# Optimization experiments

Measured on AMD Instinct MI355X. Metric: run time of the kernel, lower is better.

## Reference

```python
import jax, jax.numpy as jnp
import numpy as np

N_NODES = 100000
N_EDGES = 1600000
IN_FEATS, N_HIDDEN, N_CLASSES = 128, 128, 40


def _sage_layer(h, src, dst, W_self, W_neigh, b):
    # DGL SAGEConv (mean): fc_self(h) + fc_neigh(mean_{u in N_in(v)} h_u)
    msg = h[src]  # [E, F] gather of source-node features
    summed = jax.ops.segment_sum(msg, dst, num_segments=N_NODES)  # [N, F]
    deg = jax.ops.segment_sum(jnp.ones((src.shape[0], 1), h.dtype), dst,
                              num_segments=N_NODES)  # [N, 1] in-degree
    h_neigh = summed / jnp.maximum(deg, 1.0)
    return h @ W_self + b + h_neigh @ W_neigh


def setup_inputs() -> dict:
    key = jax.random.key(0)
    ks = jax.random.split(key, 12)
    inputs = jax.random.normal(ks[0], (N_NODES, IN_FEATS), dtype=jnp.float32)
    src = jax.random.randint(ks[1], (N_EDGES,), 0, N_NODES, dtype=jnp.int64)
    dst = jax.random.randint(ks[2], (N_EDGES,), 0, N_NODES, dtype=jnp.int64)

    def lin(k, fi, fo):
        return jax.random.normal(k, (fi, fo), dtype=jnp.float32) / np.sqrt(fi)

    return {
        "inputs": inputs, "src": src, "dst": dst,
        "W_self0": lin(ks[3], IN_FEATS, N_HIDDEN),
        "W_neigh0": lin(ks[4], IN_FEATS, N_HIDDEN),
        "b0": jnp.zeros((N_HIDDEN,), jnp.float32),
        "W_self1": lin(ks[5], N_HIDDEN, N_HIDDEN),
        "W_neigh1": lin(ks[6], N_HIDDEN, N_HIDDEN),
        "b1": jnp.zeros((N_HIDDEN,), jnp.float32),
        "W_self2": lin(ks[7], N_HIDDEN, N_CLASSES),
        "W_neigh2": lin(ks[8], N_HIDDEN, N_CLASSES),
        "b2": jnp.zeros((N_CLASSES,), jnp.float32),
    }


def reference(inputs, src, dst, W_self0, W_neigh0, b0, W_self1, W_neigh1, b1,
              W_self2, W_neigh2, b2):
    # dropout p=0.0 -> identity
    h = _sage_layer(inputs, src, dst, W_self0, W_neigh0, b0)
    h = jax.nn.relu(h)
    h = _sage_layer(h, src, dst, W_self1, W_neigh1, b1)
    h = jax.nn.relu(h)
    h = _sage_layer(h, src, dst, W_self2, W_neigh2, b2)
    return h
```

## Files before the change

### kernel.cpp

```cpp
#include <hip/hip_runtime.h>


#define F_IN 128
#define SCAN_CHUNK 1024

typedef __attribute__((ext_vector_type(8))) short bf16x8;
typedef __attribute__((ext_vector_type(4))) float f32x4;

__device__ __forceinline__ unsigned short f32_to_bf16_rne(float x) {
    unsigned int u = __float_as_uint(x);
    unsigned int r = u + 0x7FFFu + ((u >> 16) & 1u);
    return (unsigned short)(r >> 16);
}
__device__ __forceinline__ float bf16_bits_to_f32(unsigned short h) {
    return __uint_as_float(((unsigned int)h) << 16);
}


__global__ __launch_bounds__(256) void count_deg_kernel(
    const int* __restrict__ dst, int* __restrict__ cnt, int E) {
    int i = blockIdx.x * 256 + threadIdx.x;
    if (i < E) atomicAdd(&cnt[dst[i]], 1);
}

__global__ __launch_bounds__(256) void scan_part1(
    const int* __restrict__ cnt, int* __restrict__ bsum, int n) {
    __shared__ int red[4];
    int base = blockIdx.x * SCAN_CHUNK + threadIdx.x * 4;
    int s = 0;
    if (base + 4 <= n) {
        int4 v = *(const int4*)&cnt[base];
        s = v.x + v.y + v.z + v.w;
    } else {
        for (int j = 0; j < 4; ++j) if (base + j < n) s += cnt[base + j];
    }
    for (int off = 32; off > 0; off >>= 1) s += __shfl_down(s, off, 64);
    if ((threadIdx.x & 63) == 0) red[threadIdx.x >> 6] = s;
    __syncthreads();
    if (threadIdx.x == 0)
        bsum[blockIdx.x] = red[0] + red[1] + red[2] + red[3];
}

__global__ __launch_bounds__(256) void scan_part2(int* __restrict__ bsum, int nb) {
    __shared__ int tmp[256];
    int t = threadIdx.x;
    tmp[t] = (t < nb) ? bsum[t] : 0;
    __syncthreads();
    for (int off = 1; off < 256; off <<= 1) {
        int x = tmp[t];
        int add = (t >= off) ? tmp[t - off] : 0;
        __syncthreads();
        tmp[t] = x + add;
        __syncthreads();
    }
    if (t < nb) bsum[t] = (t == 0) ? 0 : tmp[t - 1];
}

__global__ __launch_bounds__(256) void scan_part3(
    const int* __restrict__ cnt, const int* __restrict__ bsum,
    int* __restrict__ row_ptr, int n, int E) {
    __shared__ int tsum[256];
    int t = threadIdx.x;
    int base = blockIdx.x * SCAN_CHUNK + t * 4;
    int c[4];
    int s = 0;
    #pragma unroll
    for (int j = 0; j < 4; ++j) {
        int idx = base + j;
        c[j] = (idx < n) ? cnt[idx] : 0;
        s += c[j];
    }
    tsum[t] = s;
    __syncthreads();
    for (int off = 1; off < 256; off <<= 1) {
        int x = tsum[t];
        int add = (t >= off) ? tsum[t - off] : 0;
        __syncthreads();
        tsum[t] = x + add;
        __syncthreads();
    }
    int p = bsum[blockIdx.x] + ((t == 0) ? 0 : tsum[t - 1]);
    #pragma unroll
    for (int j = 0; j < 4; ++j) {
        int idx = base + j;
        if (idx < n) { row_ptr[idx] = p; p += c[j]; }
    }
    if (blockIdx.x == 0 && t == 0) row_ptr[n] = E;
}

__global__ __launch_bounds__(256) void fill_kernel(
    const int* __restrict__ src, const int* __restrict__ dst,
    const int* __restrict__ row_ptr, int* __restrict__ cursor,
    int* __restrict__ col, int E) {
    int i = blockIdx.x * 256 + threadIdx.x;
    if (i < E) {
        int d = dst[i];
        int pos = atomicAdd(&cursor[d], 1);
        col[row_ptr[d] + pos] = src[i];
    }
}

__global__ __launch_bounds__(256) void aggregate_kernel(
    const float* __restrict__ h, const int* __restrict__ row_ptr,
    const int* __restrict__ col, float* __restrict__ hn, int n) {
    int g = (blockIdx.x * 256 + threadIdx.x) >> 5;
    int lane = threadIdx.x & 31;
    if (g >= n) return;
    int s = row_ptr[g], e = row_ptr[g + 1];
    const float4* h4 = (const float4*)h;
    float4 acc = make_float4(0.f, 0.f, 0.f, 0.f);
    int i = s;
    for (; i + 3 < e; i += 4) {
        int u0 = col[i], u1 = col[i + 1], u2 = col[i + 2], u3 = col[i + 3];
        float4 x0 = h4[(size_t)u0 * 32 + lane];
        float4 x1 = h4[(size_t)u1 * 32 + lane];
        float4 x2 = h4[(size_t)u2 * 32 + lane];
        float4 x3 = h4[(size_t)u3 * 32 + lane];
        acc.x += (x0.x + x1.x) + (x2.x + x3.x);
        acc.y += (x0.y + x1.y) + (x2.y + x3.y);
        acc.z += (x0.z + x1.z) + (x2.z + x3.z);
        acc.w += (x0.w + x1.w) + (x2.w + x3.w);
    }
    for (; i < e; ++i) {
        int u = col[i];
        float4 x = h4[(size_t)u * 32 + lane];
        acc.x += x.x; acc.y += x.y; acc.z += x.z; acc.w += x.w;
    }
    float inv = 1.f / fmaxf((float)(e - s), 1.f);
    float4 r = make_float4(acc.x * inv, acc.y * inv, acc.z * inv, acc.w * inv);
    ((float4*)hn)[(size_t)g * 32 + lane] = r;
}

__global__ __launch_bounds__(256) void wsplit_kernel(
    const float* __restrict__ Ws, const float* __restrict__ Wn,
    unsigned short* __restrict__ hi, unsigned short* __restrict__ lo,
    int fo, int fopad) {
    int i = blockIdx.x * 256 + threadIdx.x;
    if (i >= fopad * 256) return;
    int c = i >> 8, k = i & 255;
    float v = 0.f;
    if (c < fo) v = (k < 128) ? Ws[(size_t)k * fo + c] : Wn[(size_t)(k - 128) * fo + c];
    unsigned short h = f32_to_bf16_rne(v);
    float hf = bf16_bits_to_f32(h);
    unsigned short l = f32_to_bf16_rne(v - hf);
    hi[i] = h; lo[i] = l;
}

template <int NT, bool RELU>
__global__ __launch_bounds__(256) void gemm_mfma_kernel(
    const float* __restrict__ A, const float* __restrict__ An,
    const unsigned short* __restrict__ Wt_hi,
    const unsigned short* __restrict__ Wt_lo,
    const float* __restrict__ bias, float* __restrict__ out,
    int n, int fo) {
    int wid  = threadIdx.x >> 6;
    int lane = threadIdx.x & 63;
    int r16  = lane & 15;
    int kg   = lane >> 4;
    int Rbase = blockIdx.x * 64 + wid * 16;

    f32x4 acc[NT];
    #pragma unroll
    for (int ct = 0; ct < NT; ++ct) acc[ct] = (f32x4){0.f, 0.f, 0.f, 0.f};

    int arow = Rbase + r16;
    if (arow > n - 1) arow = n - 1;

    #pragma unroll
    for (int kstep = 0; kstep < 8; ++kstep) {
        const float* srcp = (kstep < 4) ? A : An;
        int koff = (kstep & 3) * 32 + kg * 8;
        const float* p = srcp + (size_t)arow * F_IN + koff;
        float4 v0 = *(const float4*)p;
        float4 v1 = *(const float4*)(p + 4);

        bf16x8 ahi, alo;
        {
            float va0 = v0.x, va1 = v0.y, va2 = v0.z, va3 = v0.w;
            float va4 = v1.x, va5 = v1.y, va6 = v1.z, va7 = v1.w;
            unsigned short h0 = f32_to_bf16_rne(va0), h1 = f32_to_bf16_rne(va1);
            unsigned short h2 = f32_to_bf16_rne(va2), h3 = f32_to_bf16_rne(va3);
            unsigned short h4 = f32_to_bf16_rne(va4), h5 = f32_to_bf16_rne(va5);
            unsigned short h6 = f32_to_bf16_rne(va6), h7 = f32_to_bf16_rne(va7);
            ahi[0] = (short)h0; ahi[1] = (short)h1; ahi[2] = (short)h2; ahi[3] = (short)h3;
            ahi[4] = (short)h4; ahi[5] = (short)h5; ahi[6] = (short)h6; ahi[7] = (short)h7;
            alo[0] = (short)f32_to_bf16_rne(va0 - bf16_bits_to_f32(h0));
            alo[1] = (short)f32_to_bf16_rne(va1 - bf16_bits_to_f32(h1));
            alo[2] = (short)f32_to_bf16_rne(va2 - bf16_bits_to_f32(h2));
            alo[3] = (short)f32_to_bf16_rne(va3 - bf16_bits_to_f32(h3));
            alo[4] = (short)f32_to_bf16_rne(va4 - bf16_bits_to_f32(h4));
            alo[5] = (short)f32_to_bf16_rne(va5 - bf16_bits_to_f32(h5));
            alo[6] = (short)f32_to_bf16_rne(va6 - bf16_bits_to_f32(h6));
            alo[7] = (short)f32_to_bf16_rne(va7 - bf16_bits_to_f32(h7));
        }

        int wkoff = kstep * 32 + kg * 8;
        #pragma unroll
        for (int ct = 0; ct < NT; ++ct) {
            int c = ct * 16 + r16;
            bf16x8 whi = *(const bf16x8*)(Wt_hi + (size_t)c * 256 + wkoff);
            bf16x8 wlo = *(const bf16x8*)(Wt_lo + (size_t)c * 256 + wkoff);
            acc[ct] = __builtin_amdgcn_mfma_f32_16x16x32_bf16(ahi, whi, acc[ct], 0, 0, 0);
            acc[ct] = __builtin_amdgcn_mfma_f32_16x16x32_bf16(alo, whi, acc[ct], 0, 0, 0);
            acc[ct] = __builtin_amdgcn_mfma_f32_16x16x32_bf16(ahi, wlo, acc[ct], 0, 0, 0);
        }
    }

    #pragma unroll
    for (int ct = 0; ct < NT; ++ct) {
        int c = ct * 16 + r16;
        #pragma unroll
        for (int i = 0; i < 4; ++i) {
            int node = Rbase + kg * 4 + i;
            if (node < n && c < fo) {
                float v = acc[ct][i] + bias[c];
                if (RELU) v = fmaxf(v, 0.f);
                out[(size_t)node * fo + c] = v;
            }
        }
    }
}

static inline size_t align256(size_t x) { return (x + 255) & ~(size_t)255; }

extern "C" void kernel_launch(void* const* d_in, const int* in_sizes, int n_in,
                              void* d_out, int out_size, void* d_ws, size_t ws_size,
                              hipStream_t stream) {
    const float* inputs = (const float*)d_in[0];
    const int* src = (const int*)d_in[1];
    const int* dst = (const int*)d_in[2];
    const float* Ws0 = (const float*)d_in[3];
    const float* Wn0 = (const float*)d_in[4];
    const float* b0  = (const float*)d_in[5];
    const float* Ws1 = (const float*)d_in[6];
    const float* Wn1 = (const float*)d_in[7];
    const float* b1  = (const float*)d_in[8];
    const float* Ws2 = (const float*)d_in[9];
    const float* Wn2 = (const float*)d_in[10];
    const float* b2  = (const float*)d_in[11];

    const int N = in_sizes[0] / F_IN;
    const int E = in_sizes[1];

    char* ws = (char*)d_ws;
    size_t off = 0;
    size_t off_cnt    = off; off += align256((size_t)N * 4);
    size_t off_cursor = off; off += align256((size_t)N * 4);
    size_t zero_bytes = off;
    size_t off_rowptr = off; off += align256(((size_t)N + 1) * 4);
    size_t off_bsum   = off; off += align256(1024 * 4);
    size_t off_col    = off; off += align256((size_t)E * 4);
    size_t off_hneigh = off; off += align256((size_t)N * F_IN * 4);
    size_t off_bufA   = off; off += align256((size_t)N * F_IN * 4);
    size_t off_bufB   = off; off += align256((size_t)N * F_IN * 4);
    size_t off_wt0h   = off; off += align256(128 * 256 * 2);
    size_t off_wt0l   = off; off += align256(128 * 256 * 2);
    size_t off_wt1h   = off; off += align256(128 * 256 * 2);
    size_t off_wt1l   = off; off += align256(128 * 256 * 2);
    size_t off_wt2h   = off; off += align256(48 * 256 * 2);
    size_t off_wt2l   = off; off += align256(48 * 256 * 2);
    (void)ws_size;

    int*   cnt    = (int*)(ws + off_cnt);
    int*   cursor = (int*)(ws + off_cursor);
    int*   rowptr = (int*)(ws + off_rowptr);
    int*   bsum   = (int*)(ws + off_bsum);
    int*   col    = (int*)(ws + off_col);
    float* hneigh = (float*)(ws + off_hneigh);
    float* bufA   = (float*)(ws + off_bufA);
    float* bufB   = (float*)(ws + off_bufB);
    unsigned short* wt0h = (unsigned short*)(ws + off_wt0h);
    unsigned short* wt0l = (unsigned short*)(ws + off_wt0l);
    unsigned short* wt1h = (unsigned short*)(ws + off_wt1h);
    unsigned short* wt1l = (unsigned short*)(ws + off_wt1l);
    unsigned short* wt2h = (unsigned short*)(ws + off_wt2h);
    unsigned short* wt2l = (unsigned short*)(ws + off_wt2l);
    float* out    = (float*)d_out;

    hipMemsetAsync(ws, 0, zero_bytes, stream);

    int eb = (E + 255) / 256;
    int nb = (N + SCAN_CHUNK - 1) / SCAN_CHUNK;

    count_deg_kernel<<<eb, 256, 0, stream>>>(dst, cnt, E);
    scan_part1<<<nb, 256, 0, stream>>>(cnt, bsum, N);
    scan_part2<<<1, 256, 0, stream>>>(bsum, nb);
    scan_part3<<<nb, 256, 0, stream>>>(cnt, bsum, rowptr, N, E);
    fill_kernel<<<eb, 256, 0, stream>>>(src, dst, rowptr, cursor, col, E);

    wsplit_kernel<<<(128 * 256) / 256, 256, 0, stream>>>(Ws0, Wn0, wt0h, wt0l, 128, 128);
    wsplit_kernel<<<(128 * 256) / 256, 256, 0, stream>>>(Ws1, Wn1, wt1h, wt1l, 128, 128);
    wsplit_kernel<<<(48 * 256) / 256, 256, 0, stream>>>(Ws2, Wn2, wt2h, wt2l, 40, 48);

    int ab = (N * 32 + 255) / 256;
    int gb = (N + 63) / 64;

    aggregate_kernel<<<ab, 256, 0, stream>>>(inputs, rowptr, col, hneigh, N);
    gemm_mfma_kernel<8, true><<<gb, 256, 0, stream>>>(
        inputs, hneigh, wt0h, wt0l, b0, bufA, N, 128);

    aggregate_kernel<<<ab, 256, 0, stream>>>(bufA, rowptr, col, hneigh, N);
    gemm_mfma_kernel<8, true><<<gb, 256, 0, stream>>>(
        bufA, hneigh, wt1h, wt1l, b1, bufB, N, 128);

    aggregate_kernel<<<ab, 256, 0, stream>>>(bufB, rowptr, col, hneigh, N);
    gemm_mfma_kernel<3, false><<<gb, 256, 0, stream>>>(
        bufB, hneigh, wt2h, wt2l, b2, out, N, 40);
}
```

Baseline: 909.9 us.

## Pre-split activations into bf16 hi/lo and use persistent weight-stationary MFMA GEMM

Activations are now converted to bf16 hi/lo pairs once: inputs by a new split kernel, neighbour means inside the aggregate kernel, and layer outputs in the GEMM epilogue. The GEMM becomes a persistent 512-thread kernel where each wave keeps its weight column tile in registers and loops over row tiles. This removes per-tile weight reloads and repeated fp32-to-bf16 splitting in the GEMM. The cost is extra hi/lo buffers and extra writes, and aggregation still reads fp32 outputs.

After: 912.8 us. Within noise of the previous version (+0.3%).

```diff
diff --git a/kernel.cpp b/kernel.cpp
--- a/kernel.cpp
+++ b/kernel.cpp
@@ -100,9 +100,33 @@
     }
 }
 
+__global__ __launch_bounds__(256) void asplit_kernel(
+    const float* __restrict__ in, unsigned short* __restrict__ hi,
+    unsigned short* __restrict__ lo, int total8) {
+    int i = blockIdx.x * 256 + threadIdx.x;
+    if (i >= total8) return;
+    const float4* p = (const float4*)in;
+    float4 a = p[2 * i], b = p[2 * i + 1];
+    float v[8] = {a.x, a.y, a.z, a.w, b.x, b.y, b.z, b.w};
+    unsigned int h[8], l[8];
+    #pragma unroll
+    for (int j = 0; j < 8; ++j) {
+        h[j] = f32_to_bf16_rne(v[j]);
+        l[j] = f32_to_bf16_rne(v[j] - bf16_bits_to_f32((unsigned short)h[j]));
+    }
+    uint4 H, L;
+    H.x = h[0] | (h[1] << 16); H.y = h[2] | (h[3] << 16);
+    H.z = h[4] | (h[5] << 16); H.w = h[6] | (h[7] << 16);
+    L.x = l[0] | (l[1] << 16); L.y = l[2] | (l[3] << 16);
+    L.z = l[4] | (l[5] << 16); L.w = l[6] | (l[7] << 16);
+    ((uint4*)hi)[i] = H;
+    ((uint4*)lo)[i] = L;
+}
+
 __global__ __launch_bounds__(256) void aggregate_kernel(
     const float* __restrict__ h, const int* __restrict__ row_ptr,
-    const int* __restrict__ col, float* __restrict__ hn, int n) {
+    const int* __restrict__ col, unsigned short* __restrict__ hn_hi,
+    unsigned short* __restrict__ hn_lo, int n) {
     int g = (blockIdx.x * 256 + threadIdx.x) >> 5;
     int lane = threadIdx.x & 31;
     if (g >= n) return;
@@ -127,8 +151,18 @@
         acc.x += x.x; acc.y += x.y; acc.z += x.z; acc.w += x.w;
     }
     float inv = 1.f / fmaxf((float)(e - s), 1.f);
-    float4 r = make_float4(acc.x * inv, acc.y * inv, acc.z * inv, acc.w * inv);
-    ((float4*)hn)[(size_t)g * 32 + lane] = r;
+    float r[4] = {acc.x * inv, acc.y * inv, acc.z * inv, acc.w * inv};
+    unsigned int hh[4], ll[4];
+    #pragma unroll
+    for (int j = 0; j < 4; ++j) {
+        hh[j] = f32_to_bf16_rne(r[j]);
+        ll[j] = f32_to_bf16_rne(r[j] - bf16_bits_to_f32((unsigned short)hh[j]));
+    }
+    uint2 H, L;
+    H.x = hh[0] | (hh[1] << 16); H.y = hh[2] | (hh[3] << 16);
+    L.x = ll[0] | (ll[1] << 16); L.y = ll[2] | (ll[3] << 16);
+    *(uint2*)(hn_hi + (size_t)g * 128 + lane * 4) = H;
+    *(uint2*)(hn_lo + (size_t)g * 128 + lane * 4) = L;
 }
 
 __global__ __launch_bounds__(256) void wsplit_kernel(
@@ -141,87 +175,81 @@
     float v = 0.f;
     if (c < fo) v = (k < 128) ? Ws[(size_t)k * fo + c] : Wn[(size_t)(k - 128) * fo + c];
     unsigned short h = f32_to_bf16_rne(v);
-    float hf = bf16_bits_to_f32(h);
-    unsigned short l = f32_to_bf16_rne(v - hf);
+    unsigned short l = f32_to_bf16_rne(v - bf16_bits_to_f32(h));
     hi[i] = h; lo[i] = l;
 }
 
-template <int NT, bool RELU>
-__global__ __launch_bounds__(256) void gemm_mfma_kernel(
-    const float* __restrict__ A, const float* __restrict__ An,
-    const unsigned short* __restrict__ Wt_hi,
-    const unsigned short* __restrict__ Wt_lo,
+template <int NCT, bool RELU, bool WSPLIT>
+__global__ __launch_bounds__(512) void gemm_pw_kernel(
+    const unsigned short* __restrict__ Shi, const unsigned short* __restrict__ Slo,
+    const unsigned short* __restrict__ Nhi, const unsigned short* __restrict__ Nlo,
+    const unsigned short* __restrict__ Whi, const unsigned short* __restrict__ Wlo,
     const float* __restrict__ bias, float* __restrict__ out,
+    unsigned short* __restrict__ Ohi, unsigned short* __restrict__ Olo,
     int n, int fo) {
-    int wid  = threadIdx.x >> 6;
-    int lane = threadIdx.x & 63;
-    int r16  = lane & 15;
-    int kg   = lane >> 4;
-    int Rbase = blockIdx.x * 64 + wid * 16;
-
-    f32x4 acc[NT];
-    #pragma unroll
-    for (int ct = 0; ct < NT; ++ct) acc[ct] = (f32x4){0.f, 0.f, 0.f, 0.f};
-
-    int arow = Rbase + r16;
-    if (arow > n - 1) arow = n - 1;
-
-    #pragma unroll
-    for (int kstep = 0; kstep < 8; ++kstep) {
-        const float* srcp = (kstep < 4) ? A : An;
-        int koff = (kstep & 3) * 32 + kg * 8;
-        const float* p = srcp + (size_t)arow * F_IN + koff;
-        float4 v0 = *(const float4*)p;
-        float4 v1 = *(const float4*)(p + 4);
-
-        bf16x8 ahi, alo;
-        {
-            float va0 = v0.x, va1 = v0.y, va2 = v0.z, va3 = v0.w;
-            float va4 = v1.x, va5 = v1.y, va6 = v1.z, va7 = v1.w;
-            unsigned short h0 = f32_to_bf16_rne(va0), h1 = f32_to_bf16_rne(va1);
-            unsigned short h2 = f32_to_bf16_rne(va2), h3 = f32_to_bf16_rne(va3);
-            unsigned short h4 = f32_to_bf16_rne(va4), h5 = f32_to_bf16_rne(va5);
-            unsigned short h6 = f32_to_bf16_rne(va6), h7 = f32_to_bf16_rne(va7);
-            ahi[0] = (short)h0; ahi[1] = (short)h1; ahi[2] = (short)h2; ahi[3] = (short)h3;
-            ahi[4] = (short)h4; ahi[5] = (short)h5; ahi[6] = (short)h6; ahi[7] = (short)h7;
-            alo[0] = (short)f32_to_bf16_rne(va0 - bf16_bits_to_f32(h0));
-            alo[1] = (short)f32_to_bf16_rne(va1 - bf16_bits_to_f32(h1));
-            alo[2] = (short)f32_to_bf16_rne(va2 - bf16_bits_to_f32(h2));
-            alo[3] = (short)f32_to_bf16_rne(va3 - bf16_bits_to_f32(h3));
-            alo[4] = (short)f32_to_bf16_rne(va4 - bf16_bits_to_f32(h4));
-            alo[5] = (short)f32_to_bf16_rne(va5 - bf16_bits_to_f32(h5));
-            alo[6] = (short)f32_to_bf16_rne(va6 - bf16_bits_to_f32(h6));
-            alo[7] = (short)f32_to_bf16_rne(va7 - bf16_bits_to_f32(h7));
+    constexpr int RG = 8 / NCT;
+    constexpr int BR = 32 * RG;
+    int wid = threadIdx.x >> 6, lane = threadIdx.x & 63;
+    int r16 = lane & 15, kg = lane >> 4;
+    int ct = wid & (NCT - 1), rg = wid / NCT;
+    int c = ct * 16 + r16;
+    float bv = (c < fo) ? bias[c] : 0.f;
+
+    bf16x8 wh[8], wl[8];
+    #pragma unroll
+    for (int ks = 0; ks < 8; ++ks) {
+        wh[ks] = *(const bf16x8*)(Whi + (size_t)c * 256 + ks * 32 + kg * 8);
+        wl[ks] = *(const bf16x8*)(Wlo + (size_t)c * 256 + ks * 32 + kg * 8);
+    }
+
+    int ntiles = (n + BR - 1) / BR;
+    for (int tt = blockIdx.x; tt < ntiles; tt += gridDim.x) {
+        int rowbase = tt * BR + rg * 32;
+        int ar0 = rowbase + r16;      if (ar0 > n - 1) ar0 = n - 1;
+        int ar1 = rowbase + 16 + r16; if (ar1 > n - 1) ar1 = n - 1;
+        f32x4 acc0 = (f32x4){0.f, 0.f, 0.f, 0.f};
+        f32x4 acc1 = (f32x4){0.f, 0.f, 0.f, 0.f};
+        #pragma unroll
+        for (int ks = 0; ks < 8; ++ks) {
+            const unsigned short* hs = (ks < 4) ? Shi : Nhi;
+            const unsigned short* ls = (ks < 4) ? Slo : Nlo;
+            size_t o0 = (size_t)ar0 * 128 + (ks & 3) * 32 + kg * 8;
+            size_t o1 = (size_t)ar1 * 128 + (ks & 3) * 32 + kg * 8;
+            bf16x8 ah0 = *(const bf16x8*)(hs + o0);
+            bf16x8 al0 = *(const bf16x8*)(ls + o0);
+            bf16x8 ah1 = *(const bf16x8*)(hs + o1);
+            bf16x8 al1 = *(const bf16x8*)(ls + o1);
+            acc0 = __builtin_amdgcn_mfma_f32_16x16x32_bf16(ah0, wh[ks], acc0, 0, 0, 0);
+            acc1 = __builtin_amdgcn_mfma_f32_16x16x32_bf16(ah1, wh[ks], acc1, 0, 0, 0);
+            acc0 = __builtin_amdgcn_mfma_f32_16x16x32_bf16(al0, wh[ks], acc0, 0, 0, 0);
+            acc1 = __builtin_amdgcn_mfma_f32_16x16x32_bf16(al1, wh[ks], acc1, 0, 0, 0);
+            acc0 = __builtin_amdgcn_mfma_f32_16x16x32_bf16(ah0, wl[ks], acc0, 0, 0, 0);
+            acc1 = __builtin_amdgcn_mfma_f32_16x16x32_bf16(ah1, wl[ks], acc1, 0, 0, 0);
         }
-
-        int wkoff = kstep * 32 + kg * 8;
         #pragma unroll
-        for (int ct = 0; ct < NT; ++ct) {
-            int c = ct * 16 + r16;
-            bf16x8 whi = *(const bf16x8*)(Wt_hi + (size_t)c * 256 + wkoff);
-            bf16x8 wlo = *(const bf16x8*)(Wt_lo + (size_t)c * 256 + wkoff);
-            acc[ct] = __builtin_amdgcn_mfma_f32_16x16x32_bf16(ahi, whi, acc[ct], 0, 0, 0);
-            acc[ct] = __builtin_amdgcn_mfma_f32_16x16x32_bf16(alo, whi, acc[ct], 0, 0, 0);
-            acc[ct] = __builtin_amdgcn_mfma_f32_16x16x32_bf16(ahi, wlo, acc[ct], 0, 0, 0);
-        }
-    }
-
-    #pragma unroll
-    for (int ct = 0; ct < NT; ++ct) {
-        int c = ct * 16 + r16;
-        #pragma unroll
-        for (int i = 0; i < 4; ++i) {
-            int node = Rbase + kg * 4 + i;
-            if (node < n && c < fo) {
-                float v = acc[ct][i] + bias[c];
-                if (RELU) v = fmaxf(v, 0.f);
-                out[(size_t)node * fo + c] = v;
+        for (int m = 0; m < 2; ++m) {
+            f32x4 acc = m ? acc1 : acc0;
+            #pragma unroll
+            for (int i = 0; i < 4; ++i) {
+                int node = rowbase + m * 16 + kg * 4 + i;
+                if (node < n && c < fo) {
+                    float v = acc[i] + bv;
+                    if (RELU) v = fmaxf(v, 0.f);
+                    out[(size_t)node * fo + c] = v;
+                    if (WSPLIT) {
+                        unsigned short hh = f32_to_bf16_rne(v);
+                        Ohi[(size_t)node * 128 + c] = hh;
+                        Olo[(size_t)node * 128 + c] =
+                            f32_to_bf16_rne(v - bf16_bits_to_f32(hh));
+                    }
+                }
             }
         }
     }
 }
 
 static inline size_t align256(size_t x) { return (x + 255) & ~(size_t)255; }
+static inline int imin(int a, int b) { return a < b ? a : b; }
 
 extern "C" void kernel_launch(void* const* d_in, const int* in_sizes, int n_in,
                               void* d_out, int out_size, void* d_ws, size_t ws_size,
@@ -250,15 +278,20 @@
     size_t off_rowptr = off; off += align256(((size_t)N + 1) * 4);
     size_t off_bsum   = off; off += align256(1024 * 4);
     size_t off_col    = off; off += align256((size_t)E * 4);
-    size_t off_hneigh = off; off += align256((size_t)N * F_IN * 4);
     size_t off_bufA   = off; off += align256((size_t)N * F_IN * 4);
     size_t off_bufB   = off; off += align256((size_t)N * F_IN * 4);
+    size_t off_s0h    = off; off += align256((size_t)N * F_IN * 2);
+    size_t off_s0l    = off; off += align256((size_t)N * F_IN * 2);
+    size_t off_s1h    = off; off += align256((size_t)N * F_IN * 2);
+    size_t off_s1l    = off; off += align256((size_t)N * F_IN * 2);
+    size_t off_hnh    = off; off += align256((size_t)N * F_IN * 2);
+    size_t off_hnl    = off; off += align256((size_t)N * F_IN * 2);
     size_t off_wt0h   = off; off += align256(128 * 256 * 2);
     size_t off_wt0l   = off; off += align256(128 * 256 * 2);
     size_t off_wt1h   = off; off += align256(128 * 256 * 2);
     size_t off_wt1l   = off; off += align256(128 * 256 * 2);
-    size_t off_wt2h   = off; off += align256(48 * 256 * 2);
-    size_t off_wt2l   = off; off += align256(48 * 256 * 2);
+    size_t off_wt2h   = off; off += align256(64 * 256 * 2);
+    size_t off_wt2l   = off; off += align256(64 * 256 * 2);
     (void)ws_size;
 
     int*   cnt    = (int*)(ws + off_cnt);
@@ -266,9 +299,14 @@
     int*   rowptr = (int*)(ws + off_rowptr);
     int*   bsum   = (int*)(ws + off_bsum);
     int*   col    = (int*)(ws + off_col);
-    float* hneigh = (float*)(ws + off_hneigh);
     float* bufA   = (float*)(ws + off_bufA);
     float* bufB   = (float*)(ws + off_bufB);
+    unsigned short* s0h = (unsigned short*)(ws + off_s0h);
+    unsigned short* s0l = (unsigned short*)(ws + off_s0l);
+    unsigned short* s1h = (unsigned short*)(ws + off_s1h);
+    unsigned short* s1l = (unsigned short*)(ws + off_s1l);
+    unsigned short* hnh = (unsigned short*)(ws + off_hnh);
+    unsigned short* hnl = (unsigned short*)(ws + off_hnl);
     unsigned short* wt0h = (unsigned short*)(ws + off_wt0h);
     unsigned short* wt0l = (unsigned short*)(ws + off_wt0l);
     unsigned short* wt1h = (unsigned short*)(ws + off_wt1h);
@@ -288,22 +326,26 @@
     scan_part3<<<nb, 256, 0, stream>>>(cnt, bsum, rowptr, N, E);
     fill_kernel<<<eb, 256, 0, stream>>>(src, dst, rowptr, cursor, col, E);
 
+    int total8 = N * (F_IN / 8);
+    asplit_kernel<<<(total8 + 255) / 256, 256, 0, stream>>>(inputs, s0h, s0l, total8);
     wsplit_kernel<<<(128 * 256) / 256, 256, 0, stream>>>(Ws0, Wn0, wt0h, wt0l, 128, 128);
     wsplit_kernel<<<(128 * 256) / 256, 256, 0, stream>>>(Ws1, Wn1, wt1h, wt1l, 128, 128);
-    wsplit_kernel<<<(48 * 256) / 256, 256, 0, stream>>>(Ws2, Wn2, wt2h, wt2l, 40, 48);
+    wsplit_kernel<<<(64 * 256) / 256, 256, 0, stream>>>(Ws2, Wn2, wt2h, wt2l, 40, 64);
 
     int ab = (N * 32 + 255) / 256;
-    int gb = (N + 63) / 64;
-
-    aggregate_kernel<<<ab, 256, 0, stream>>>(inputs, rowptr, col, hneigh, N);
-    gemm_mfma_kernel<8, true><<<gb, 256, 0, stream>>>(
-        inputs, hneigh, wt0h, wt0l, b0, bufA, N, 128);
-
-    aggregate_kernel<<<ab, 256, 0, stream>>>(bufA, rowptr, col, hneigh, N);
-    gemm_mfma_kernel<8, true><<<gb, 256, 0, stream>>>(
-        bufA, hneigh, wt1h, wt1l, b1, bufB, N, 128);
-
-    aggregate_kernel<<<ab, 256, 0, stream>>>(bufB, rowptr, col, hneigh, N);
-    gemm_mfma_kernel<3, false><<<gb, 256, 0, stream>>>(
-        bufB, hneigh, wt2h, wt2l, b2, out, N, 40);
-}
+    int g01 = imin((N + 31) / 32, 1024);
+    int g2  = imin((N + 63) / 64, 1024);
+
+    aggregate_kernel<<<ab, 256, 0, stream>>>(inputs, rowptr, col, hnh, hnl, N);
+    gemm_pw_kernel<8, true, true><<<g01, 512, 0, stream>>>(
+        s0h, s0l, hnh, hnl, wt0h, wt0l, b0, bufA, s1h, s1l, N, 128);
+
+    aggregate_kernel<<<ab, 256, 0, stream>>>(bufA, rowptr, col, hnh, hnl, N);
+    gemm_pw_kernel<8, true, true><<<g01, 512, 0, stream>>>(
+        s1h, s1l, hnh, hnl, wt1h, wt1l, b1, bufB, s0h, s0l, N, 128);
+
+    aggregate_kernel<<<ab, 256, 0, stream>>>(bufB, rowptr, col, hnh, hnl, N);
+    gemm_pw_kernel<4, false, false><<<g2, 512, 0, stream>>>(
+        s0h, s0l, hnh, hnl, wt2h, wt2l, b2, out, (unsigned short*)nullptr,
+        (unsigned short*)nullptr, N, 40);
+}
```
